# Kernel optimization log

Measured on AMD Instinct MI355X. Metric: run time of the kernel, lower is better.

## Reference

```python
import jax, jax.numpy as jnp
import numpy as np


def setup_inputs() -> dict:
    key = jax.random.key(0)
    k1, k2 = jax.random.split(key)
    n, c, H, W = 8, 16, 512, 512
    pred = jax.random.normal(k1, (n, c, H, W), dtype=jnp.float32)
    target = jax.random.randint(k2, (n, H, W), 0, c, dtype=jnp.int64)
    weights = jnp.ones((n, 1, H, W), dtype=jnp.float32)  # ignored by the module
    return {"pred": pred, "target": target, "weights": weights}


def reference(pred, target, weights):
    # pred: [n,c,H,W] logits; target: [n,H,W] int class ids; weights arg is ignored
    n, c, H, W = pred.shape
    # Global (whole-batch) per-class pixel counts -> inverse-frequency weights.
    counts = jnp.zeros((c,), dtype=pred.dtype).at[target.reshape(-1)].add(1.0)
    w_class = jnp.where(counts > 0, 1.0 / (counts * c), 0.0)  # [c]
    w = w_class[target]  # [n,H,W] per-pixel weight (constant w.r.t. pred)
    # log-softmax gathered at target class per pixel
    logp = jax.nn.log_softmax(pred, axis=1)  # [n,c,H,W]
    lp_t = jnp.take_along_axis(logp, target[:, None, :, :], axis=1)[:, 0]  # [n,H,W]
    num = (lp_t * w).reshape(n, -1).sum(axis=1)  # [n]
    den = w.reshape(n, -1).sum(axis=1)           # [n]
    return -(num / den).mean()
```

## Files before the change

### kernel.cpp

```cpp
#include <hip/hip_runtime.h>
#include <stdint.h>

#define NIMG 8
#define NCLS 16
#define HW   262144
#define PXB  1024
#define NBLK 2048

__device__ __forceinline__ void g2lds16(const float* g, float* l) {
    __builtin_amdgcn_global_load_lds(
        (const __attribute__((address_space(1))) unsigned int*)g,
        (__attribute__((address_space(3))) unsigned int*)l,
        16, 0, 0);
}

__global__ __launch_bounds__(256) void dwce_main(const float* __restrict__ pred,
                                                 const int* __restrict__ tgt,
                                                 float* __restrict__ partials) {
    __shared__ float tile[NCLS * PXB];
    __shared__ float s_bin[32];
    const int tid = threadIdx.x;
    if (tid < 32) s_bin[tid] = 0.0f;

    const int b = blockIdx.x;
    const long long px0 = (long long)b * PXB;
    const int n_img = (int)(px0 >> 18);
    const int hw0   = (int)(px0 & (HW - 1));
    const float* base = pred + (size_t)n_img * NCLS * HW + hw0;

    const int w    = tid >> 6;
    const int lane = tid & 63;
    const int woff = w * 256 + lane * 4;

#pragma unroll
    for (int c = 0; c < NCLS; ++c)
        g2lds16(base + (size_t)c * HW + woff, &tile[c * PXB + woff]);

    const int4 t4 = *(const int4*)(tgt + px0 + tid * 4);

    __syncthreads();

    const int p = tid * 4;

    float4 m  = make_float4(-3.0e38f, -3.0e38f, -3.0e38f, -3.0e38f);
    float4 xt = make_float4(0.f, 0.f, 0.f, 0.f);
#pragma unroll
    for (int c = 0; c < NCLS; ++c) {
        const float4 v = *(const float4*)&tile[c * PXB + p];
        m.x = fmaxf(m.x, v.x);
        m.y = fmaxf(m.y, v.y);
        m.z = fmaxf(m.z, v.z);
        m.w = fmaxf(m.w, v.w);
        if (t4.x == c) xt.x = v.x;
        if (t4.y == c) xt.y = v.y;
        if (t4.z == c) xt.z = v.z;
        if (t4.w == c) xt.w = v.w;
    }

    float4 s = make_float4(0.f, 0.f, 0.f, 0.f);
#pragma unroll
    for (int c = 0; c < NCLS; ++c) {
        const float4 v = *(const float4*)&tile[c * PXB + p];
        s.x += __expf(v.x - m.x);
        s.y += __expf(v.y - m.y);
        s.z += __expf(v.z - m.z);
        s.w += __expf(v.w - m.w);
    }

    const float lp0 = xt.x - (m.x + __logf(s.x));
    const float lp1 = xt.y - (m.y + __logf(s.y));
    const float lp2 = xt.z - (m.z + __logf(s.z));
    const float lp3 = xt.w - (m.w + __logf(s.w));

    atomicAdd(&s_bin[t4.x], lp0);
    atomicAdd(&s_bin[t4.y], lp1);
    atomicAdd(&s_bin[t4.z], lp2);
    atomicAdd(&s_bin[t4.w], lp3);
    atomicAdd(&s_bin[16 + t4.x], 1.0f);
    atomicAdd(&s_bin[16 + t4.y], 1.0f);
    atomicAdd(&s_bin[16 + t4.z], 1.0f);
    atomicAdd(&s_bin[16 + t4.w], 1.0f);

    __syncthreads();
    if (tid < 32)
        partials[(size_t)tid * NBLK + b] = s_bin[tid];
}

__global__ __launch_bounds__(256) void dwce_final(const float* __restrict__ ws,
                                                  float* __restrict__ out) {
    __shared__ float tot[32][NIMG];
    __shared__ float wcl[NCLS];
    __shared__ float ratio[NIMG];
    const int tid = threadIdx.x;
    const int c = tid >> 3;
    const int n = tid & 7;

    const float4* p = (const float4*)(ws + (size_t)c * NBLK + n * 256);
    float4 a = make_float4(0.f, 0.f, 0.f, 0.f);
#pragma unroll 8
    for (int k = 0; k < 64; ++k) {
        float4 q = p[k];
        a.x += q.x; a.y += q.y; a.z += q.z; a.w += q.w;
    }
    tot[c][n] = (a.x + a.y) + (a.z + a.w);
    __syncthreads();

    if (tid < NCLS) {
        float g = 0.f;
#pragma unroll
        for (int i = 0; i < NIMG; ++i) g += tot[NCLS + tid][i];
        wcl[tid] = (g > 0.f) ? 1.0f / (g * (float)NCLS) : 0.0f;
    }
    __syncthreads();
    if (tid < NIMG) {
        float num = 0.f, den = 0.f;
#pragma unroll
        for (int c2 = 0; c2 < NCLS; ++c2) {
            num += tot[c2][tid] * wcl[c2];
            den += tot[NCLS + c2][tid] * wcl[c2];
        }
        ratio[tid] = num / den;
    }
    __syncthreads();
    if (tid == 0) {
        float r = 0.f;
#pragma unroll
        for (int i = 0; i < NIMG; ++i) r += ratio[i];
        out[0] = -r * (1.0f / (float)NIMG);
    }
}

extern "C" void kernel_launch(void* const* d_in, const int* in_sizes, int n_in,
                              void* d_out, int out_size, void* d_ws, size_t ws_size,
                              hipStream_t stream) {
    const float* pred = (const float*)d_in[0];
    const int*   tgt  = (const int*)d_in[1];
    float* out = (float*)d_out;
    float* ws  = (float*)d_ws;

    dwce_main<<<NBLK, 256, 0, stream>>>(pred, tgt, ws);
    dwce_final<<<1, 256, 0, stream>>>(ws, out);
}
```

Before: 206.8 us.

## Replace LDS staging with direct register loads and two-chunk online softmax

```diff
diff --git a/kernel.cpp b/kernel.cpp
--- a/kernel.cpp
+++ b/kernel.cpp
@@ -1,71 +1,92 @@
 #include <hip/hip_runtime.h>
-#include <stdint.h>
 
 #define NIMG 8
 #define NCLS 16
 #define HW   262144
-#define PXB  1024
 #define NBLK 2048
 
-__device__ __forceinline__ void g2lds16(const float* g, float* l) {
-    __builtin_amdgcn_global_load_lds(
-        (const __attribute__((address_space(1))) unsigned int*)g,
-        (__attribute__((address_space(3))) unsigned int*)l,
-        16, 0, 0);
-}
-
-__global__ __launch_bounds__(256) void dwce_main(const float* __restrict__ pred,
-                                                 const int* __restrict__ tgt,
-                                                 float* __restrict__ partials) {
-    __shared__ float tile[NCLS * PXB];
+__global__ __launch_bounds__(256, 8) void dwce_main(const float* __restrict__ pred,
+                                                    const int* __restrict__ tgt,
+                                                    float* __restrict__ partials) {
     __shared__ float s_bin[32];
     const int tid = threadIdx.x;
     if (tid < 32) s_bin[tid] = 0.0f;
-
-    const int b = blockIdx.x;
-    const long long px0 = (long long)b * PXB;
-    const int n_img = (int)(px0 >> 18);
-    const int hw0   = (int)(px0 & (HW - 1));
-    const float* base = pred + (size_t)n_img * NCLS * HW + hw0;
-
-    const int w    = tid >> 6;
-    const int lane = tid & 63;
-    const int woff = w * 256 + lane * 4;
-
-#pragma unroll
-    for (int c = 0; c < NCLS; ++c)
-        g2lds16(base + (size_t)c * HW + woff, &tile[c * PXB + woff]);
-
-    const int4 t4 = *(const int4*)(tgt + px0 + tid * 4);
-
     __syncthreads();
 
-    const int p = tid * 4;
+    const int gid = blockIdx.x * 256 + tid;
+    const long long p0 = (long long)gid * 4;
+    const int n_img = (int)(p0 >> 18);
+    const int hw    = (int)(p0 & (HW - 1));
+    const float* base = pred + (size_t)n_img * NCLS * HW + hw;
 
-    float4 m  = make_float4(-3.0e38f, -3.0e38f, -3.0e38f, -3.0e38f);
+    const int4 t4 = *(const int4*)(tgt + p0);
+
+    float4 m1, s1, m2, s2;
     float4 xt = make_float4(0.f, 0.f, 0.f, 0.f);
+
+    {
+        float4 v[8];
 #pragma unroll
-    for (int c = 0; c < NCLS; ++c) {
-        const float4 v = *(const float4*)&tile[c * PXB + p];
-        m.x = fmaxf(m.x, v.x);
-        m.y = fmaxf(m.y, v.y);
-        m.z = fmaxf(m.z, v.z);
-        m.w = fmaxf(m.w, v.w);
-        if (t4.x == c) xt.x = v.x;
-        if (t4.y == c) xt.y = v.y;
-        if (t4.z == c) xt.z = v.z;
-        if (t4.w == c) xt.w = v.w;
+        for (int j = 0; j < 8; ++j)
+            v[j] = *(const float4*)(base + (size_t)j * HW);
+        m1 = v[0];
+#pragma unroll
+        for (int j = 1; j < 8; ++j) {
+            m1.x = fmaxf(m1.x, v[j].x);
+            m1.y = fmaxf(m1.y, v[j].y);
+            m1.z = fmaxf(m1.z, v[j].z);
+            m1.w = fmaxf(m1.w, v[j].w);
+        }
+        s1 = make_float4(0.f, 0.f, 0.f, 0.f);
+#pragma unroll
+        for (int j = 0; j < 8; ++j) {
+            s1.x += __expf(v[j].x - m1.x);
+            s1.y += __expf(v[j].y - m1.y);
+            s1.z += __expf(v[j].z - m1.z);
+            s1.w += __expf(v[j].w - m1.w);
+            if (t4.x == j) xt.x = v[j].x;
+            if (t4.y == j) xt.y = v[j].y;
+            if (t4.z == j) xt.z = v[j].z;
+            if (t4.w == j) xt.w = v[j].w;
+        }
+    }
+    {
+        float4 v[8];
+#pragma unroll
+        for (int j = 0; j < 8; ++j)
+            v[j] = *(const float4*)(base + (size_t)(8 + j) * HW);
+        m2 = v[0];
+#pragma unroll
+        for (int j = 1; j < 8; ++j) {
+            m2.x = fmaxf(m2.x, v[j].x);
+            m2.y = fmaxf(m2.y, v[j].y);
+            m2.z = fmaxf(m2.z, v[j].z);
+            m2.w = fmaxf(m2.w, v[j].w);
+        }
+        s2 = make_float4(0.f, 0.f, 0.f, 0.f);
+#pragma unroll
+        for (int j = 0; j < 8; ++j) {
+            s2.x += __expf(v[j].x - m2.x);
+            s2.y += __expf(v[j].y - m2.y);
+            s2.z += __expf(v[j].z - m2.z);
+            s2.w += __expf(v[j].w - m2.w);
+            if (t4.x == 8 + j) xt.x = v[j].x;
+            if (t4.y == 8 + j) xt.y = v[j].y;
+            if (t4.z == 8 + j) xt.z = v[j].z;
+            if (t4.w == 8 + j) xt.w = v[j].w;
+        }
     }
 
-    float4 s = make_float4(0.f, 0.f, 0.f, 0.f);
-#pragma unroll
-    for (int c = 0; c < NCLS; ++c) {
-        const float4 v = *(const float4*)&tile[c * PXB + p];
-        s.x += __expf(v.x - m.x);
-        s.y += __expf(v.y - m.y);
-        s.z += __expf(v.z - m.z);
-        s.w += __expf(v.w - m.w);
-    }
+    float4 m;
+    m.x = fmaxf(m1.x, m2.x);
+    m.y = fmaxf(m1.y, m2.y);
+    m.z = fmaxf(m1.z, m2.z);
+    m.w = fmaxf(m1.w, m2.w);
+    float4 s;
+    s.x = s1.x * __expf(m1.x - m.x) + s2.x * __expf(m2.x - m.x);
+    s.y = s1.y * __expf(m1.y - m.y) + s2.y * __expf(m2.y - m.y);
+    s.z = s1.z * __expf(m1.z - m.z) + s2.z * __expf(m2.z - m.z);
+    s.w = s1.w * __expf(m1.w - m.w) + s2.w * __expf(m2.w - m.w);
 
     const float lp0 = xt.x - (m.x + __logf(s.x));
     const float lp1 = xt.y - (m.y + __logf(s.y));
@@ -83,7 +104,7 @@
 
     __syncthreads();
     if (tid < 32)
-        partials[(size_t)tid * NBLK + b] = s_bin[tid];
+        partials[(size_t)tid * NBLK + blockIdx.x] = s_bin[tid];
 }
 
 __global__ __launch_bounds__(256) void dwce_final(const float* __restrict__ ws,
```

New measurement: 235.0 us. +13.7%, slower.

## Replace LDS staging with direct register loads and online softmax

Applied to the files above, without the earlier changes.

```diff
diff --git a/kernel.cpp b/kernel.cpp
--- a/kernel.cpp
+++ b/kernel.cpp
@@ -1,70 +1,56 @@
 #include <hip/hip_runtime.h>
-#include <stdint.h>
 
 #define NIMG 8
 #define NCLS 16
 #define HW   262144
-#define PXB  1024
 #define NBLK 2048
 
-__device__ __forceinline__ void g2lds16(const float* g, float* l) {
-    __builtin_amdgcn_global_load_lds(
-        (const __attribute__((address_space(1))) unsigned int*)g,
-        (__attribute__((address_space(3))) unsigned int*)l,
-        16, 0, 0);
-}
-
-__global__ __launch_bounds__(256) void dwce_main(const float* __restrict__ pred,
-                                                 const int* __restrict__ tgt,
-                                                 float* __restrict__ partials) {
-    __shared__ float tile[NCLS * PXB];
+__global__ __launch_bounds__(256, 8) void dwce_main(const float* __restrict__ pred,
+                                                    const int* __restrict__ tgt,
+                                                    float* __restrict__ partials) {
     __shared__ float s_bin[32];
     const int tid = threadIdx.x;
     if (tid < 32) s_bin[tid] = 0.0f;
+    __syncthreads();
 
-    const int b = blockIdx.x;
-    const long long px0 = (long long)b * PXB;
-    const int n_img = (int)(px0 >> 18);
-    const int hw0   = (int)(px0 & (HW - 1));
-    const float* base = pred + (size_t)n_img * NCLS * HW + hw0;
+    const int gid = blockIdx.x * 256 + tid;
+    const long long p0 = (long long)gid * 4;
+    const int n_img = (int)(p0 >> 18);
+    const int hw    = (int)(p0 & (HW - 1));
+    const float* base = pred + (size_t)n_img * NCLS * HW + hw;
 
-    const int w    = tid >> 6;
-    const int lane = tid & 63;
-    const int woff = w * 256 + lane * 4;
+    const int4 t4 = *(const int4*)(tgt + p0);
+
+    float4 v0 = *(const float4*)(base);
+    float4 v1 = *(const float4*)(base + HW);
+
+    float4 m  = make_float4(-3.0e38f, -3.0e38f, -3.0e38f, -3.0e38f);
+    float4 s  = make_float4(0.f, 0.f, 0.f, 0.f);
+    float4 xt = make_float4(0.f, 0.f, 0.f, 0.f);
 
 #pragma unroll
-    for (int c = 0; c < NCLS; ++c)
-        g2lds16(base + (size_t)c * HW + woff, &tile[c * PXB + woff]);
+    for (int c = 0; c < NCLS; ++c) {
+        float4 vn = make_float4(0.f, 0.f, 0.f, 0.f);
+        if (c + 2 < NCLS)
+            vn = *(const float4*)(base + (size_t)(c + 2) * HW);
 
-    const int4 t4 = *(const int4*)(tgt + px0 + tid * 4);
+        float4 mn;
+        mn.x = fmaxf(m.x, v0.x);
+        mn.y = fmaxf(m.y, v0.y);
+        mn.z = fmaxf(m.z, v0.z);
+        mn.w = fmaxf(m.w, v0.w);
+        s.x = s.x * __expf(m.x - mn.x) + __expf(v0.x - mn.x);
+        s.y = s.y * __expf(m.y - mn.y) + __expf(v0.y - mn.y);
+        s.z = s.z * __expf(m.z - mn.z) + __expf(v0.z - mn.z);
+        s.w = s.w * __expf(m.w - mn.w) + __expf(v0.w - mn.w);
+        m = mn;
+        if (t4.x == c) xt.x = v0.x;
+        if (t4.y == c) xt.y = v0.y;
+        if (t4.z == c) xt.z = v0.z;
+        if (t4.w == c) xt.w = v0.w;
 
-    __syncthreads();
-
-    const int p = tid * 4;
-
-    float4 m  = make_float4(-3.0e38f, -3.0e38f, -3.0e38f, -3.0e38f);
-    float4 xt = make_float4(0.f, 0.f, 0.f, 0.f);
-#pragma unroll
-    for (int c = 0; c < NCLS; ++c) {
-        const float4 v = *(const float4*)&tile[c * PXB + p];
-        m.x = fmaxf(m.x, v.x);
-        m.y = fmaxf(m.y, v.y);
-        m.z = fmaxf(m.z, v.z);
-        m.w = fmaxf(m.w, v.w);
-        if (t4.x == c) xt.x = v.x;
-        if (t4.y == c) xt.y = v.y;
-        if (t4.z == c) xt.z = v.z;
-        if (t4.w == c) xt.w = v.w;
-    }
-
-    float4 s = make_float4(0.f, 0.f, 0.f, 0.f);
-#pragma unroll
-    for (int c = 0; c < NCLS; ++c) {
-        const float4 v = *(const float4*)&tile[c * PXB + p];
-        s.x += __expf(v.x - m.x);
-        s.y += __expf(v.y - m.y);
-        s.z += __expf(v.z - m.z);
-        s.w += __expf(v.w - m.w);
+        v0 = v1;
+        v1 = vn;
     }
 
     const float lp0 = xt.x - (m.x + __logf(s.x));
@@ -83,7 +69,7 @@
 
     __syncthreads();
     if (tid < 32)
-        partials[(size_t)tid * NBLK + b] = s_bin[tid];
+        partials[(size_t)tid * NBLK + blockIdx.x] = s_bin[tid];
 }
 
 __global__ __launch_bounds__(256) void dwce_final(const float* __restrict__ ws,
```

Measured after the change: 211.7 us. +2.4%, slower.
